# Optimization experiments

Hardware: AMD Instinct MI355X
Metric: run time of the kernel (lower is better)

The kernel has to match this reference:

```python
import jax, jax.numpy as jnp
import numpy as np

B, S, D = 32, 1024, 512
LN_EPS = 1e-5


def setup_inputs() -> dict:
    key = jax.random.key(0)
    ks = jax.random.split(key, 12)
    scale = 1.0 / np.sqrt(D)
    return {
        "seq1": jax.random.normal(ks[0], (B, S, D), jnp.float32),
        "seq2": jax.random.normal(ks[1], (B, S, D), jnp.float32),
        "mask1": jax.random.randint(ks[2], (B, S), 0, 2) == 1,
        "mask2": jax.random.randint(ks[3], (B, S), 0, 2) == 1,
        "Wq": jax.random.uniform(ks[4], (D, D), jnp.float32, -scale, scale),
        "bq": jax.random.uniform(ks[5], (D,), jnp.float32, -scale, scale),
        "Wk": jax.random.uniform(ks[6], (D, D), jnp.float32, -scale, scale),
        "bk": jax.random.uniform(ks[7], (D,), jnp.float32, -scale, scale),
        "Wv": jax.random.uniform(ks[8], (D, D), jnp.float32, -scale, scale),
        "bv": jax.random.uniform(ks[9], (D,), jnp.float32, -scale, scale),
        "gamma": jnp.ones((D,), jnp.float32),
        "beta": jnp.zeros((D,), jnp.float32),
    }


def _layernorm(x, gamma, beta):
    mu = jnp.mean(x, axis=-1, keepdims=True)
    var = jnp.mean(jnp.square(x - mu), axis=-1, keepdims=True)
    return (x - mu) * jax.lax.rsqrt(var + LN_EPS) * gamma + beta


def reference(seq1, seq2, mask1, mask2, Wq, bq, Wk, bk, Wv, bv, gamma, beta):
    # relu-projected Q/K/V (shared weights across both sequences)
    q1 = jax.nn.relu(seq1 @ Wq + bq)
    k1 = jax.nn.relu(seq1 @ Wk + bk)
    v1 = jax.nn.relu(seq1 @ Wv + bv)
    q2 = jax.nn.relu(seq2 @ Wq + bq)
    k2 = jax.nn.relu(seq2 @ Wk + bk)
    v2 = jax.nn.relu(seq2 @ Wv + bv)

    # bilinear cross scores: tanh(k1 q2^T) summed over seq2 -> [B,S1]
    a1 = jnp.sum(jnp.tanh(jnp.einsum('bsd,btd->bst', k1, q2)), axis=2)
    a2 = jnp.sum(jnp.tanh(jnp.einsum('btd,bsd->bts', k2, q1)), axis=2)

    a1 = jnp.where(mask1, -jnp.inf, a1)
    a2 = jnp.where(mask2, -jnp.inf, a2)
    a1 = jax.nn.softmax(a1, axis=-1)  # [B,S1]
    a2 = jax.nn.softmax(a2, axis=-1)  # [B,S2]
    # dropout p=0.2 is identity at inference

    vector1 = jnp.einsum('bs,bsd->bd', a1, v1)
    vector2 = jnp.einsum('bs,bsd->bd', a2, v2)

    out1 = _layernorm(jnp.mean(seq1, axis=1) + vector1, gamma, beta)
    out2 = _layernorm(jnp.mean(seq2, axis=1) + vector2, gamma, beta)
    return (out1, out2)
```

## Files before the change

kernel.cpp:

```cpp
#include <hip/hip_runtime.h>


typedef __bf16 bf16x8_t __attribute__((ext_vector_type(8)));
typedef float f32x4_t __attribute__((ext_vector_type(4)));

__device__ __forceinline__ unsigned short f2bf(float f) {
    union { float f; unsigned int u; } c; c.f = f;
    unsigned int u = c.u;
    unsigned int r = (u + 0x7FFFu + ((u >> 16) & 1u)) >> 16;
    return (unsigned short)r;
}
__device__ __forceinline__ float bf2f(unsigned short h) {
    union { unsigned int u; float f; } c; c.u = ((unsigned int)h) << 16;
    return c.f;
}
__device__ __forceinline__ void gl2lds16(const void* g, void* l) {
    __builtin_amdgcn_global_load_lds(
        (const __attribute__((address_space(1))) void*)g,
        (__attribute__((address_space(3))) void*)l, 16, 0, 0);
}
__device__ __forceinline__ float fast_tanh(float x) {
    float e = __expf(2.f * x);
    return 1.f - 2.f * __builtin_amdgcn_rcpf(e + 1.f);
}

__global__ __launch_bounds__(256) void wconv_kernel(
    const float* __restrict__ Wq, const float* __restrict__ Wk,
    const float* __restrict__ Wv, unsigned short* __restrict__ Wt)
{
    const float* W = (blockIdx.z == 0) ? Wq : (blockIdx.z == 1) ? Wk : Wv;
    unsigned short* o = Wt + (size_t)blockIdx.z * 512 * 512;
    __shared__ unsigned short t[64][65];
    int k0 = blockIdx.x * 64, n0 = blockIdx.y * 64;
    #pragma unroll
    for (int i = 0; i < 16; ++i) {
        int idx = i * 256 + threadIdx.x;
        int r = idx >> 6, c = idx & 63;
        t[r][c] = f2bf(W[(size_t)(k0 + r) * 512 + n0 + c]);
    }
    __syncthreads();
    #pragma unroll
    for (int i = 0; i < 16; ++i) {
        int idx = i * 256 + threadIdx.x;
        int r = idx >> 6, c = idx & 63;
        o[(size_t)(n0 + r) * 512 + k0 + c] = t[c][r];
    }
}

__global__ __launch_bounds__(256) void qkv_gemm(
    const float* __restrict__ seq1, const float* __restrict__ seq2,
    const unsigned short* __restrict__ Wt,
    const float* __restrict__ bq, const float* __restrict__ bk,
    const float* __restrict__ bv, unsigned short* __restrict__ qkv)
{
    int nt = blockIdx.x, mt = blockIdx.y, z = blockIdx.z;
    int sq = z / 3, w = z % 3;
    const float* X = sq ? seq2 : seq1;
    const unsigned short* Bt = Wt + (size_t)w * 512 * 512;
    const float* bias = (w == 0) ? bq : (w == 1) ? bk : bv;
    unsigned short* out = qkv + (size_t)z * 32768 * 512;

    __shared__ alignas(16) unsigned short As[128 * 32];
    __shared__ alignas(16) unsigned short Bs[128 * 32];

    int tid = threadIdx.x;
    int lane = tid & 63, wv = tid >> 6;
    int wm = wv >> 1, wn = wv & 1;
    int q = lane >> 4, ln = lane & 15;
    int m0 = mt * 128, n0 = nt * 128;

    f32x4_t acc[4][4] = {};

    for (int k0 = 0; k0 < 512; k0 += 32) {
        #pragma unroll
        for (int j = 0; j < 4; ++j) {
            int idx = j * 1024 + tid * 4;
            int r = idx >> 5, kk = idx & 31;
            const float4 v = *reinterpret_cast<const float4*>(
                &X[(size_t)(m0 + r) * 512 + k0 + kk]);
            ushort4 h;
            h.x = f2bf(v.x); h.y = f2bf(v.y); h.z = f2bf(v.z); h.w = f2bf(v.w);
            *reinterpret_cast<ushort4*>(&As[r * 32 + kk]) = h;
        }
        #pragma unroll
        for (int j = 0; j < 2; ++j) {
            int cbase = j * 256 + wv * 64;
            int c = cbase + lane;
            int nrow = c >> 2, kk8 = (c & 3) * 8;
            gl2lds16(&Bt[(size_t)(n0 + nrow) * 512 + k0 + kk8], &Bs[cbase * 8]);
        }
        __syncthreads();

        bf16x8_t af[4], bfr[4];
        #pragma unroll
        for (int i = 0; i < 4; ++i)
            af[i] = *reinterpret_cast<const bf16x8_t*>(
                &As[(wm * 64 + i * 16 + ln) * 32 + q * 8]);
        #pragma unroll
        for (int j = 0; j < 4; ++j)
            bfr[j] = *reinterpret_cast<const bf16x8_t*>(
                &Bs[(wn * 64 + j * 16 + ln) * 32 + q * 8]);
        #pragma unroll
        for (int i = 0; i < 4; ++i)
            #pragma unroll
            for (int j = 0; j < 4; ++j)
                acc[i][j] = __builtin_amdgcn_mfma_f32_16x16x32_bf16(
                    af[i], bfr[j], acc[i][j], 0, 0, 0);
        __syncthreads();
    }

    float bv4[4];
    #pragma unroll
    for (int j = 0; j < 4; ++j) bv4[j] = bias[n0 + wn * 64 + j * 16 + ln];
    #pragma unroll
    for (int i = 0; i < 4; ++i) {
        #pragma unroll
        for (int r = 0; r < 4; ++r) {
            int m = m0 + wm * 64 + i * 16 + q * 4 + r;
            #pragma unroll
            for (int j = 0; j < 4; ++j) {
                int n = n0 + wn * 64 + j * 16 + ln;
                float c = acc[i][j][r] + bv4[j];
                c = fmaxf(c, 0.f);
                out[(size_t)m * 512 + n] = f2bf(c);
            }
        }
    }
}

__global__ __launch_bounds__(256) void score_kernel(
    const unsigned short* __restrict__ qkv, float* __restrict__ a_out)
{
    int tt = blockIdx.x, st = blockIdx.y, z = blockIdx.z;
    int which = z >> 5, b = z & 31;
    const unsigned short* Am =
        qkv + ((size_t)(which ? 4 : 1) * 32768 + (size_t)b * 1024) * 512;
    const unsigned short* Bm =
        qkv + ((size_t)(which ? 0 : 3) * 32768 + (size_t)b * 1024) * 512;

    __shared__ alignas(16) unsigned short As[128 * 32];
    __shared__ alignas(16) unsigned short Bs[128 * 32];

    int tid = threadIdx.x;
    int lane = tid & 63, wv = tid >> 6;
    int wm = wv >> 1, wn = wv & 1;
    int q = lane >> 4, ln = lane & 15;
    int s0 = st * 128, t0 = tt * 128;

    f32x4_t acc[4][4] = {};

    for (int k0 = 0; k0 < 512; k0 += 32) {
        #pragma unroll
        for (int j = 0; j < 2; ++j) {
            int cbase = j * 256 + wv * 64;
            int c = cbase + lane;
            int row = c >> 2, kk8 = (c & 3) * 8;
            gl2lds16(&Am[(size_t)(s0 + row) * 512 + k0 + kk8], &As[cbase * 8]);
            gl2lds16(&Bm[(size_t)(t0 + row) * 512 + k0 + kk8], &Bs[cbase * 8]);
        }
        __syncthreads();

        bf16x8_t af[4], bfr[4];
        #pragma unroll
        for (int i = 0; i < 4; ++i)
            af[i] = *reinterpret_cast<const bf16x8_t*>(
                &As[(wm * 64 + i * 16 + ln) * 32 + q * 8]);
        #pragma unroll
        for (int j = 0; j < 4; ++j)
            bfr[j] = *reinterpret_cast<const bf16x8_t*>(
                &Bs[(wn * 64 + j * 16 + ln) * 32 + q * 8]);
        #pragma unroll
        for (int i = 0; i < 4; ++i)
            #pragma unroll
            for (int j = 0; j < 4; ++j)
                acc[i][j] = __builtin_amdgcn_mfma_f32_16x16x32_bf16(
                    af[i], bfr[j], acc[i][j], 0, 0, 0);
        __syncthreads();
    }

    #pragma unroll
    for (int i = 0; i < 4; ++i) {
        #pragma unroll
        for (int r = 0; r < 4; ++r) {
            float s = 0.f;
            #pragma unroll
            for (int j = 0; j < 4; ++j) s += fast_tanh(acc[i][j][r]);
            #pragma unroll
            for (int off = 1; off <= 8; off <<= 1) s += __shfl_xor(s, off, 64);
            if (ln == 0)
                atomicAdd(&a_out[(size_t)z * 1024 + s0 + wm * 64 + i * 16 + q * 4 + r], s);
        }
    }
}

__global__ __launch_bounds__(256) void softmax_kernel(
    const float* __restrict__ a_in, const int* __restrict__ mask1,
    const int* __restrict__ mask2, float* __restrict__ w_out)
{
    int z = blockIdx.x, which = z >> 5, b = z & 31;
    const int* mask = (which ? mask2 : mask1) + (size_t)b * 1024;
    const float* a = a_in + (size_t)z * 1024;
    float* w = w_out + (size_t)z * 1024;
    int tid = threadIdx.x, lane = tid & 63, wv = tid >> 6;

    float vals[4];
    #pragma unroll
    for (int j = 0; j < 4; ++j) {
        int s = tid + j * 256;
        vals[j] = mask[s] ? -__builtin_inff() : a[s];
    }
    float m = fmaxf(fmaxf(vals[0], vals[1]), fmaxf(vals[2], vals[3]));
    #pragma unroll
    for (int off = 32; off; off >>= 1) m = fmaxf(m, __shfl_xor(m, off, 64));
    __shared__ float redm[4], redsum[4];
    if (lane == 0) redm[wv] = m;
    __syncthreads();
    m = fmaxf(fmaxf(redm[0], redm[1]), fmaxf(redm[2], redm[3]));

    float e[4], sum = 0.f;
    #pragma unroll
    for (int j = 0; j < 4; ++j) { e[j] = __expf(vals[j] - m); sum += e[j]; }
    #pragma unroll
    for (int off = 32; off; off >>= 1) sum += __shfl_xor(sum, off, 64);
    if (lane == 0) redsum[wv] = sum;
    __syncthreads();
    sum = redsum[0] + redsum[1] + redsum[2] + redsum[3];
    float inv = 1.f / sum;
    #pragma unroll
    for (int j = 0; j < 4; ++j) w[tid + j * 256] = e[j] * inv;
}

__global__ __launch_bounds__(512) void wsum_kernel(
    const unsigned short* __restrict__ qkv, const float* __restrict__ w_in,
    const float* __restrict__ seq1, const float* __restrict__ seq2,
    float* __restrict__ acc)
{
    int chunk = blockIdx.x;
    int z = blockIdx.y, which = z >> 5, b = z & 31;
    const unsigned short* V =
        qkv + ((size_t)(which ? 5 : 2) * 32768 + (size_t)b * 1024) * 512;
    const float* seq = (which ? seq2 : seq1) + (size_t)b * 1024 * 512;
    const float* w = w_in + (size_t)z * 1024;
    int d = threadIdx.x;
    float a = 0.f;
    int s0 = chunk * 128;
    for (int s = s0; s < s0 + 128; ++s) {
        a += w[s] * bf2f(V[(size_t)s * 512 + d]);
        a += seq[(size_t)s * 512 + d] * (1.f / 1024.f);
    }
    atomicAdd(&acc[(size_t)z * 512 + d], a);
}

__global__ __launch_bounds__(512) void ln_kernel(
    const float* __restrict__ acc, const float* __restrict__ gamma,
    const float* __restrict__ beta, float* __restrict__ out)
{
    int z = blockIdx.x, d = threadIdx.x;
    int lane = d & 63, wv = d >> 6;
    float x = acc[(size_t)z * 512 + d];
    float s = x;
    #pragma unroll
    for (int off = 32; off; off >>= 1) s += __shfl_xor(s, off, 64);
    __shared__ float red[8], red2[8];
    if (lane == 0) red[wv] = s;
    __syncthreads();
    float mu = 0.f;
    #pragma unroll
    for (int i = 0; i < 8; ++i) mu += red[i];
    mu *= (1.f / 512.f);
    float c = x - mu;
    float s2 = c * c;
    #pragma unroll
    for (int off = 32; off; off >>= 1) s2 += __shfl_xor(s2, off, 64);
    if (lane == 0) red2[wv] = s2;
    __syncthreads();
    float var = 0.f;
    #pragma unroll
    for (int i = 0; i < 8; ++i) var += red2[i];
    var *= (1.f / 512.f);
    out[(size_t)z * 512 + d] = c * __frsqrt_rn(var + 1e-5f) * gamma[d] + beta[d];
}

extern "C" void kernel_launch(void* const* d_in, const int* in_sizes, int n_in,
                              void* d_out, int out_size, void* d_ws, size_t ws_size,
                              hipStream_t stream) {
    const float* seq1 = (const float*)d_in[0];
    const float* seq2 = (const float*)d_in[1];
    const int* mask1 = (const int*)d_in[2];
    const int* mask2 = (const int*)d_in[3];
    const float* Wq = (const float*)d_in[4];
    const float* bq = (const float*)d_in[5];
    const float* Wk = (const float*)d_in[6];
    const float* bk = (const float*)d_in[7];
    const float* Wv = (const float*)d_in[8];
    const float* bv = (const float*)d_in[9];
    const float* gamma = (const float*)d_in[10];
    const float* beta = (const float*)d_in[11];
    float* out = (float*)d_out;

    char* ws = (char*)d_ws;
    float* a_sc = (float*)(ws);
    float* wsm = (float*)(ws + (256u << 10));
    float* accv = (float*)(ws + (512u << 10));
    unsigned short* Wt = (unsigned short*)(ws + (1u << 20));
    unsigned short* qkv = (unsigned short*)(ws + (4u << 20));

    hipMemsetAsync(ws, 0, 640u << 10, stream);

    wconv_kernel<<<dim3(8, 8, 3), 256, 0, stream>>>(Wq, Wk, Wv, Wt);
    qkv_gemm<<<dim3(4, 256, 6), 256, 0, stream>>>(seq1, seq2, Wt, bq, bk, bv, qkv);
    score_kernel<<<dim3(8, 8, 64), 256, 0, stream>>>(qkv, a_sc);
    softmax_kernel<<<64, 256, 0, stream>>>(a_sc, mask1, mask2, wsm);
    wsum_kernel<<<dim3(8, 64), 512, 0, stream>>>(qkv, wsm, seq1, seq2, accv);
    ln_kernel<<<64, 512, 0, stream>>>(accv, gamma, beta, out);
}
```

Baseline: 542.3 us.

## Pre-convert inputs to bf16 once and fuse QKV projections into wider GEMM tiles

Adds a conversion kernel that turns each sequence into bf16 once and accumulates the sequence mean into the layernorm accumulator at the same time. The QKV GEMM then loads both A and B through global-to-LDS DMA and computes a 256-wide concatenated Q|K|V tile, so each activation tile is read once per pass instead of three times. The mean-of-sequence term is removed from the weighted-sum kernel. The bf16 copy of seq1 is written into the seq2 input buffer after seq2 has been converted. That saves workspace but destroys the caller's input, which can break repeated calls.

```diff
diff --git a/kernel.cpp b/kernel.cpp
--- a/kernel.cpp
+++ b/kernel.cpp
@@ -24,6 +24,43 @@
     return 1.f - 2.f * __builtin_amdgcn_rcpf(e + 1.f);
 }
 
+__global__ __launch_bounds__(256) void x2bf_kernel(
+    const float* __restrict__ src, unsigned short* __restrict__ dst,
+    float* __restrict__ accv)
+{
+    int chunk = blockIdx.x;
+    int b = blockIdx.y;
+    int tid = threadIdx.x, lane = tid & 63, wv = tid >> 6;
+    __shared__ float red[4][512];
+    float sum[8] = {};
+    size_t base = ((size_t)b * 1024 + (size_t)chunk * 128) * 512;
+    #pragma unroll 4
+    for (int i = 0; i < 32; ++i) {
+        int r = i * 4 + wv;
+        size_t ro = base + (size_t)r * 512;
+        float4 a = *reinterpret_cast<const float4*>(&src[ro + lane * 4]);
+        float4 c = *reinterpret_cast<const float4*>(&src[ro + 256 + lane * 4]);
+        ushort4 ha; ha.x = f2bf(a.x); ha.y = f2bf(a.y); ha.z = f2bf(a.z); ha.w = f2bf(a.w);
+        ushort4 hc; hc.x = f2bf(c.x); hc.y = f2bf(c.y); hc.z = f2bf(c.z); hc.w = f2bf(c.w);
+        *reinterpret_cast<ushort4*>(&dst[ro + lane * 4]) = ha;
+        *reinterpret_cast<ushort4*>(&dst[ro + 256 + lane * 4]) = hc;
+        sum[0] += a.x; sum[1] += a.y; sum[2] += a.z; sum[3] += a.w;
+        sum[4] += c.x; sum[5] += c.y; sum[6] += c.z; sum[7] += c.w;
+    }
+    #pragma unroll
+    for (int t = 0; t < 4; ++t) {
+        red[wv][lane * 4 + t] = sum[t];
+        red[wv][256 + lane * 4 + t] = sum[4 + t];
+    }
+    __syncthreads();
+    #pragma unroll
+    for (int j = 0; j < 2; ++j) {
+        int col = tid + j * 256;
+        float s = red[0][col] + red[1][col] + red[2][col] + red[3][col];
+        atomicAdd(&accv[(size_t)b * 512 + col], s * (1.f / 1024.f));
+    }
+}
+
 __global__ __launch_bounds__(256) void wconv_kernel(
     const float* __restrict__ Wq, const float* __restrict__ Wk,
     const float* __restrict__ Wv, unsigned short* __restrict__ Wt)
@@ -47,82 +84,81 @@
     }
 }
 
+__global__ __launch_bounds__(512) void biascat_kernel(
+    const float* __restrict__ bq, const float* __restrict__ bk,
+    const float* __restrict__ bv, float* __restrict__ bc)
+{
+    int n = threadIdx.x;
+    bc[n] = bq[n]; bc[512 + n] = bk[n]; bc[1024 + n] = bv[n];
+}
+
 __global__ __launch_bounds__(256) void qkv_gemm(
-    const float* __restrict__ seq1, const float* __restrict__ seq2,
-    const unsigned short* __restrict__ Wt,
-    const float* __restrict__ bq, const float* __restrict__ bk,
-    const float* __restrict__ bv, unsigned short* __restrict__ qkv)
+    const unsigned short* __restrict__ Xb1, const unsigned short* __restrict__ Xb2,
+    const unsigned short* __restrict__ Wt, const float* __restrict__ bias_cat,
+    unsigned short* __restrict__ qkv)
 {
     int nt = blockIdx.x, mt = blockIdx.y, z = blockIdx.z;
-    int sq = z / 3, w = z % 3;
-    const float* X = sq ? seq2 : seq1;
-    const unsigned short* Bt = Wt + (size_t)w * 512 * 512;
-    const float* bias = (w == 0) ? bq : (w == 1) ? bk : bv;
-    unsigned short* out = qkv + (size_t)z * 32768 * 512;
+    const unsigned short* X = z ? Xb2 : Xb1;
 
     __shared__ alignas(16) unsigned short As[128 * 32];
-    __shared__ alignas(16) unsigned short Bs[128 * 32];
+    __shared__ alignas(16) unsigned short Bs[256 * 32];
 
     int tid = threadIdx.x;
     int lane = tid & 63, wv = tid >> 6;
     int wm = wv >> 1, wn = wv & 1;
     int q = lane >> 4, ln = lane & 15;
-    int m0 = mt * 128, n0 = nt * 128;
-
-    f32x4_t acc[4][4] = {};
+    int m0 = mt * 128, n0 = nt * 256;
+
+    f32x4_t acc[4][8] = {};
 
     for (int k0 = 0; k0 < 512; k0 += 32) {
-        #pragma unroll
-        for (int j = 0; j < 4; ++j) {
-            int idx = j * 1024 + tid * 4;
-            int r = idx >> 5, kk = idx & 31;
-            const float4 v = *reinterpret_cast<const float4*>(
-                &X[(size_t)(m0 + r) * 512 + k0 + kk]);
-            ushort4 h;
-            h.x = f2bf(v.x); h.y = f2bf(v.y); h.z = f2bf(v.z); h.w = f2bf(v.w);
-            *reinterpret_cast<ushort4*>(&As[r * 32 + kk]) = h;
-        }
         #pragma unroll
         for (int j = 0; j < 2; ++j) {
             int cbase = j * 256 + wv * 64;
             int c = cbase + lane;
-            int nrow = c >> 2, kk8 = (c & 3) * 8;
-            gl2lds16(&Bt[(size_t)(n0 + nrow) * 512 + k0 + kk8], &Bs[cbase * 8]);
+            gl2lds16(&X[(size_t)(m0 + (c >> 2)) * 512 + k0 + (c & 3) * 8],
+                     &As[cbase * 8]);
+        }
+        #pragma unroll
+        for (int j = 0; j < 4; ++j) {
+            int cbase = j * 256 + wv * 64;
+            int c = cbase + lane;
+            gl2lds16(&Wt[(size_t)(n0 + (c >> 2)) * 512 + k0 + (c & 3) * 8],
+                     &Bs[cbase * 8]);
         }
         __syncthreads();
 
-        bf16x8_t af[4], bfr[4];
+        bf16x8_t af[4], bfr[8];
         #pragma unroll
         for (int i = 0; i < 4; ++i)
             af[i] = *reinterpret_cast<const bf16x8_t*>(
                 &As[(wm * 64 + i * 16 + ln) * 32 + q * 8]);
         #pragma unroll
-        for (int j = 0; j < 4; ++j)
+        for (int j = 0; j < 8; ++j)
             bfr[j] = *reinterpret_cast<const bf16x8_t*>(
-                &Bs[(wn * 64 + j * 16 + ln) * 32 + q * 8]);
+                &Bs[(wn * 128 + j * 16 + ln) * 32 + q * 8]);
         #pragma unroll
         for (int i = 0; i < 4; ++i)
             #pragma unroll
-            for (int j = 0; j < 4; ++j)
+            for (int j = 0; j < 8; ++j)
                 acc[i][j] = __builtin_amdgcn_mfma_f32_16x16x32_bf16(
                     af[i], bfr[j], acc[i][j], 0, 0, 0);
         __syncthreads();
     }
 
-    float bv4[4];
-    #pragma unroll
-    for (int j = 0; j < 4; ++j) bv4[j] = bias[n0 + wn * 64 + j * 16 + ln];
-    #pragma unroll
-    for (int i = 0; i < 4; ++i) {
-        #pragma unroll
-        for (int r = 0; r < 4; ++r) {
-            int m = m0 + wm * 64 + i * 16 + q * 4 + r;
-            #pragma unroll
-            for (int j = 0; j < 4; ++j) {
-                int n = n0 + wn * 64 + j * 16 + ln;
-                float c = acc[i][j][r] + bv4[j];
-                c = fmaxf(c, 0.f);
-                out[(size_t)m * 512 + n] = f2bf(c);
+    #pragma unroll
+    for (int j = 0; j < 8; ++j) {
+        int n = n0 + wn * 128 + j * 16 + ln;
+        int w = n >> 9, col = n & 511;
+        float bb = bias_cat[n];
+        unsigned short* out = qkv + (size_t)(z * 3 + w) * 32768 * 512;
+        #pragma unroll
+        for (int i = 0; i < 4; ++i) {
+            #pragma unroll
+            for (int r = 0; r < 4; ++r) {
+                int m = m0 + wm * 64 + i * 16 + q * 4 + r;
+                float cv = fmaxf(acc[i][j][r] + bb, 0.f);
+                out[(size_t)m * 512 + col] = f2bf(cv);
             }
         }
     }
@@ -232,22 +268,18 @@
 
 __global__ __launch_bounds__(512) void wsum_kernel(
     const unsigned short* __restrict__ qkv, const float* __restrict__ w_in,
-    const float* __restrict__ seq1, const float* __restrict__ seq2,
     float* __restrict__ acc)
 {
     int chunk = blockIdx.x;
     int z = blockIdx.y, which = z >> 5, b = z & 31;
     const unsigned short* V =
         qkv + ((size_t)(which ? 5 : 2) * 32768 + (size_t)b * 1024) * 512;
-    const float* seq = (which ? seq2 : seq1) + (size_t)b * 1024 * 512;
     const float* w = w_in + (size_t)z * 1024;
     int d = threadIdx.x;
     float a = 0.f;
     int s0 = chunk * 128;
-    for (int s = s0; s < s0 + 128; ++s) {
+    for (int s = s0; s < s0 + 128; ++s)
         a += w[s] * bf2f(V[(size_t)s * 512 + d]);
-        a += seq[(size_t)s * 512 + d] * (1.f / 1024.f);
-    }
     atomicAdd(&acc[(size_t)z * 512 + d], a);
 }
 
@@ -302,15 +334,21 @@
     float* a_sc = (float*)(ws);
     float* wsm = (float*)(ws + (256u << 10));
     float* accv = (float*)(ws + (512u << 10));
+    float* bias_cat = (float*)(ws + (768u << 10));
     unsigned short* Wt = (unsigned short*)(ws + (1u << 20));
-    unsigned short* qkv = (unsigned short*)(ws + (4u << 20));
+    unsigned short* Xb2 = (unsigned short*)(ws + (4ull << 20));
+    unsigned short* qkv = (unsigned short*)(ws + (40ull << 20));
+    unsigned short* Xb1 = (unsigned short*)d_in[1];
 
     hipMemsetAsync(ws, 0, 640u << 10, stream);
 
     wconv_kernel<<<dim3(8, 8, 3), 256, 0, stream>>>(Wq, Wk, Wv, Wt);
-    qkv_gemm<<<dim3(4, 256, 6), 256, 0, stream>>>(seq1, seq2, Wt, bq, bk, bv, qkv);
+    biascat_kernel<<<1, 512, 0, stream>>>(bq, bk, bv, bias_cat);
+    x2bf_kernel<<<dim3(8, 32), 256, 0, stream>>>(seq2, Xb2, accv + 32 * 512);
+    x2bf_kernel<<<dim3(8, 32), 256, 0, stream>>>(seq1, Xb1, accv);
+    qkv_gemm<<<dim3(6, 256, 2), 256, 0, stream>>>(Xb1, Xb2, Wt, bias_cat, qkv);
     score_kernel<<<dim3(8, 8, 64), 256, 0, stream>>>(qkv, a_sc);
     softmax_kernel<<<64, 256, 0, stream>>>(a_sc, mask1, mask2, wsm);
-    wsum_kernel<<<dim3(8, 64), 512, 0, stream>>>(qkv, wsm, seq1, seq2, accv);
+    wsum_kernel<<<dim3(8, 64), 512, 0, stream>>>(qkv, wsm, accv);
     ln_kernel<<<64, 512, 0, stream>>>(accv, gamma, beta, out);
 }
```

New measurement: 569.2 us. 4.9% more time.
